# Optimization experiments

Measured on AMD Instinct MI355X. Metric: run time of the kernel, lower is better.

The kernel has to match this reference:

```python
import jax, jax.numpy as jnp
import numpy as np

DIM = 256          # channel dim
WIN = 16           # window_size
PW = WIN // 2      # permuted_window_size
N = PW * PW        # tokens per window = 64
H = 8              # num_heads
KV_DIM = DIM // 2  # compressed q/k/v dim = 128
HD = KV_DIM // H   # per-head compressed dim = 16
SCALE = (DIM // H) ** (-0.5)  # NOTE: scale uses UNcompressed head dim, as in source
B = 4096           # total windows (batch * num_windows)
NW = 64            # nw_mask; B % NW == 0


def _relative_position_index():
    coords = np.stack(np.meshgrid(np.arange(PW), np.arange(PW), indexing='ij'))  # [2,PW,PW]
    cf = coords.reshape(2, -1)                          # [2, N]
    rel = cf[:, :, None] - cf[:, None, :]               # [2, N, N]
    rel = rel.transpose(1, 2, 0).copy()                 # [N, N, 2]
    rel[:, :, 0] += PW - 1
    rel[:, :, 1] += PW - 1
    rel[:, :, 0] *= 2 * PW - 1
    return jnp.asarray(rel.sum(-1), dtype=jnp.int32)    # [N, N]


def setup_inputs() -> dict:
    key = jax.random.key(0)
    ks = jax.random.split(key, 9)
    std = 0.02
    return {
        'x': jax.random.normal(ks[0], (B, N, DIM), dtype=jnp.float32),
        'mask': jax.random.normal(ks[1], (NW, N, N), dtype=jnp.float32),
        'q_w': jax.random.normal(ks[2], (KV_DIM, DIM), dtype=jnp.float32) * std,
        'q_b': jnp.zeros((KV_DIM,), dtype=jnp.float32),
        'kv_w': jax.random.normal(ks[3], (2 * KV_DIM, DIM), dtype=jnp.float32) * std,
        'kv_b': jnp.zeros((2 * KV_DIM,), dtype=jnp.float32),
        'proj_w': jax.random.normal(ks[4], (DIM, KV_DIM), dtype=jnp.float32) * std,
        'proj_b': jnp.zeros((DIM,), dtype=jnp.float32),
        'bias_table': jax.random.normal(ks[5], ((2 * PW - 1) ** 2, H), dtype=jnp.float32) * std,
        'rel_index': _relative_position_index(),
    }


def reference(x, mask, q_w, q_b, kv_w, kv_b, proj_w, proj_b, bias_table, rel_index):
    b, n, c = x.shape
    # compressed Q and KV projections
    q = (x @ q_w.T + q_b).reshape(b, n, H, HD).transpose(0, 2, 1, 3)        # [B,H,N,HD]
    kv = (x @ kv_w.T + kv_b).reshape(b, n, 2, H, HD).transpose(2, 0, 3, 1, 4)
    k, v = kv[0], kv[1]                                                     # [B,H,N,HD]
    attn = jnp.einsum('bhnd,bhmd->bhnm', q, k) * SCALE                      # [B,H,N,N]
    # relative position bias gather
    bias = bias_table[rel_index.reshape(-1)].reshape(n, n, H).transpose(2, 0, 1)  # [H,N,N]
    attn = attn + bias[None]
    # window mask add: broadcast mask over (B//NW) window-batches and heads
    attn = attn.reshape(b // NW, NW, H, n, n) + mask[None, :, None]
    attn = attn.reshape(b, H, n, n)
    attn = jax.nn.softmax(attn, axis=-1)
    out = jnp.einsum('bhnm,bhmd->bhnd', attn, v)                            # [B,H,N,HD]
    out = out.transpose(0, 2, 1, 3).reshape(b, n, KV_DIM)
    return out @ proj_w.T + proj_b                                          # [B,N,DIM]
```

## Files before the change

### kernel.cpp

```cpp
#include <hip/hip_runtime.h>


typedef unsigned short u16;
typedef short bf16x8 __attribute__((ext_vector_type(8)));
typedef short bf16x4 __attribute__((ext_vector_type(4)));
typedef float f32x4  __attribute__((ext_vector_type(4)));

__device__ __forceinline__ f32x4 mfma_bf16(bf16x8 a, bf16x8 b, f32x4 c) {
  return __builtin_amdgcn_mfma_f32_16x16x32_bf16(a, b, c, 0, 0, 0);
}
__device__ __forceinline__ f32x4 mfma16(bf16x4 a, bf16x4 b, f32x4 c) {
#if __has_builtin(__builtin_amdgcn_mfma_f32_16x16x16bf16_1k)
  return __builtin_amdgcn_mfma_f32_16x16x16bf16_1k(a, b, c, 0, 0, 0);
#else
  f32x4 d;
  asm("v_mfma_f32_16x16x16_bf16 %0, %1, %2, %3" : "=v"(d) : "v"(a), "v"(b), "v"(c));
  return d;
#endif
}

#define SCALE_F 0.1767766952966369f
#define LOG2E_F 1.4426950408889634f
#define C2F (SCALE_F * LOG2E_F)

__device__ __forceinline__ u16 f2b(float f) {
  unsigned u = __builtin_bit_cast(unsigned, f);
  u = (u + 0x7FFFu + ((u >> 16) & 1u)) >> 16;
  return (u16)u;
}
__device__ __forceinline__ float b2f(u16 h) {
  return __builtin_bit_cast(float, (unsigned)h << 16);
}
__device__ __forceinline__ float fexp2(float x) {
#if __has_builtin(__builtin_amdgcn_exp2f)
  return __builtin_amdgcn_exp2f(x);
#else
  return __expf(x * 0.6931471805599453f);
#endif
}

#define WS_WQKV   0
#define WS_WPROJ  98304
#define WS_BIASPK 131072
#define WS_MASKPK 163840
#define WS_QKVB   425984
#define WS_TOTAL  426368

__global__ void psa_prep(const float* __restrict__ qw, const float* __restrict__ qb,
                         const float* __restrict__ kvw, const float* __restrict__ kvb,
                         const float* __restrict__ projw, const float* __restrict__ bt,
                         const int* __restrict__ ri, const float* __restrict__ mask,
                         u16* __restrict__ ws) {
  int i = blockIdx.x * 256 + threadIdx.x;
  if (i < 98304) {
    int r = i >> 8, c = i & 255;
    ws[WS_WQKV + i] = f2b(r < 128 ? qw[r * 256 + c] : kvw[(r - 128) * 256 + c]);
  } else if (i < 131072) {
    int j = i - 98304;
    ws[WS_WPROJ + j] = f2b(projw[j]);
  } else if (i < 163840) {
    int j = i - 131072;
    int t = j & 15, lane = (j >> 4) & 63, w = (j >> 10) & 3, h = j >> 12;
    int row = w * 16 + (lane & 15);
    int col = (t >> 2) * 16 + ((lane >> 4) & 3) * 4 + (t & 3);
    ws[WS_BIASPK + j] = f2b(LOG2E_F * bt[ri[row * 64 + col] * 8 + h]);
  } else if (i < 425984) {
    int j = i - 163840;
    int t = j & 15, lane = (j >> 4) & 63, w = (j >> 10) & 3, nw = j >> 12;
    int row = w * 16 + (lane & 15);
    int col = (t >> 2) * 16 + ((lane >> 4) & 3) * 4 + (t & 3);
    ws[WS_MASKPK + j] = f2b(LOG2E_F * mask[(nw * 64 + row) * 64 + col]);
  } else if (i < WS_TOTAL) {
    int j = i - 425984;
    ws[WS_QKVB + j] = f2b(j < 128 ? qb[j] : kvb[j - 128]);
  }
}

__global__ __launch_bounds__(256, 3) void psa_main(
    const float* __restrict__ x, const float* __restrict__ proj_b,
    const u16* __restrict__ ws, float* __restrict__ out) {
  __shared__ __align__(16) u16 qks[64 * 264];
  __shared__ __align__(16) u16 vsm[8 * 16 * 72];

  const int win = blockIdx.x;
  const int tid = threadIdx.x;
  const int wave = tid >> 6;
  const int lane = tid & 63;
  const int quad = lane >> 4;
  const int n16  = lane & 15;
  const int nw   = win & 63;

  const f32x4 zero4 = {0.f, 0.f, 0.f, 0.f};
  const float* xw = x + (size_t)win * 16384;

  #pragma unroll
  for (int it = 0; it < 16; ++it) {
    int idx = it * 256 + tid;
    int row = idx >> 6, c4 = (idx & 63) * 4;
    float4 v = *(const float4*)(xw + row * 256 + c4);
    bf16x4 pk;
    pk[0] = (short)f2b(v.x); pk[1] = (short)f2b(v.y);
    pk[2] = (short)f2b(v.z); pk[3] = (short)f2b(v.w);
    *(bf16x4*)&qks[row * 264 + c4] = pk;
  }
  __syncthreads();

  f32x4 acc[6][4];
  #pragma unroll
  for (int nt = 0; nt < 6; ++nt)
    #pragma unroll
    for (int mt = 0; mt < 4; ++mt) acc[nt][mt] = zero4;

  const int col0 = wave * 96;
  #pragma unroll 2
  for (int kk = 0; kk < 8; ++kk) {
    bf16x8 af[4];
    #pragma unroll
    for (int mt = 0; mt < 4; ++mt)
      af[mt] = *(const bf16x8*)&qks[(mt * 16 + n16) * 264 + kk * 32 + quad * 8];
    #pragma unroll
    for (int nt = 0; nt < 6; ++nt) {
      bf16x8 bw = *(const bf16x8*)&ws[WS_WQKV + (col0 + nt * 16 + n16) * 256 + kk * 32 + quad * 8];
      #pragma unroll
      for (int mt = 0; mt < 4; ++mt) acc[nt][mt] = mfma_bf16(af[mt], bw, acc[nt][mt]);
    }
  }
  __syncthreads();

  #pragma unroll
  for (int nt = 0; nt < 6; ++nt) {
    int col = col0 + nt * 16 + n16;
    float badd = b2f(ws[WS_QKVB + col]);
    if (col < 256) {
      #pragma unroll
      for (int mt = 0; mt < 4; ++mt)
        #pragma unroll
        for (int r = 0; r < 4; ++r)
          qks[(mt * 16 + quad * 4 + r) * 264 + col] = f2b(acc[nt][mt][r] + badd);
    } else {
      int vc = col - 256, vh = vc >> 4, vd = vc & 15;
      #pragma unroll
      for (int mt = 0; mt < 4; ++mt)
        #pragma unroll
        for (int r = 0; r < 4; ++r)
          vsm[vh * 1152 + vd * 72 + mt * 16 + quad * 4 + r] = f2b(acc[nt][mt][r] + badd);
    }
  }
  __syncthreads();

  const u16* bpk = ws + WS_BIASPK + (wave * 64 + lane) * 16;
  const u16* mpk = ws + WS_MASKPK + ((nw * 4 + wave) * 64 + lane) * 16;
  bf16x8 mm0 = *(const bf16x8*)mpk;
  bf16x8 mm1 = *(const bf16x8*)(mpk + 8);

  #pragma unroll 1
  for (int h = 0; h < 8; ++h) {
    bf16x4 qf = *(const bf16x4*)&qks[(wave * 16 + n16) * 264 + h * 16 + quad * 4];
    f32x4 s[4];
    #pragma unroll
    for (int nt = 0; nt < 4; ++nt) {
      bf16x4 kf = *(const bf16x4*)&qks[(nt * 16 + n16) * 264 + 128 + h * 16 + quad * 4];
      s[nt] = mfma16(kf, qf, zero4);
    }
    bf16x8 bm0 = *(const bf16x8*)(bpk + h * 4096);
    bf16x8 bm1 = *(const bf16x8*)(bpk + h * 4096 + 8);

    float e[4][4];
    float sum = 0.f;
    #pragma unroll
    for (int nt = 0; nt < 4; ++nt)
      #pragma unroll
      for (int r = 0; r < 4; ++r) {
        int j = nt * 4 + r;
        float bv = b2f((u16)(j < 8 ? bm0[j] : bm1[j - 8]));
        float mv = b2f((u16)(j < 8 ? mm0[j] : mm1[j - 8]));
        float ev = fexp2(s[nt][r] * C2F + (bv + mv));
        e[nt][r] = ev;
        sum += ev;
      }
    sum += __shfl_xor(sum, 16);
    sum += __shfl_xor(sum, 32);
    float rinv = __builtin_amdgcn_rcpf(sum);

    bf16x4 pf[4];
    #pragma unroll
    for (int nt = 0; nt < 4; ++nt) {
      bf16x4 t;
      #pragma unroll
      for (int r = 0; r < 4; ++r) t[r] = (short)f2b(e[nt][r]);
      pf[nt] = t;
    }
    f32x4 o = zero4;
    #pragma unroll
    for (int kt = 0; kt < 4; ++kt) {
      bf16x4 vf = *(const bf16x4*)&vsm[h * 1152 + n16 * 72 + kt * 16 + quad * 4];
      o = mfma16(vf, pf[kt], o);
    }
    bf16x4 ov;
    #pragma unroll
    for (int r = 0; r < 4; ++r) ov[r] = (short)f2b(o[r] * rinv);
    *(bf16x4*)&qks[(wave * 16 + n16) * 264 + h * 16 + quad * 4] = ov;
  }
  __syncthreads();

  f32x4 po[4][4];
  #pragma unroll
  for (int nt = 0; nt < 4; ++nt)
    #pragma unroll
    for (int mt = 0; mt < 4; ++mt) po[nt][mt] = zero4;
  #pragma unroll
  for (int ks = 0; ks < 4; ++ks) {
    bf16x8 af[4];
    #pragma unroll
    for (int mt = 0; mt < 4; ++mt)
      af[mt] = *(const bf16x8*)&qks[(mt * 16 + n16) * 264 + ks * 32 + quad * 8];
    #pragma unroll
    for (int nt = 0; nt < 4; ++nt) {
      bf16x8 bw = *(const bf16x8*)&ws[WS_WPROJ + (wave * 64 + nt * 16 + n16) * 128 + ks * 32 + quad * 8];
      #pragma unroll
      for (int mt = 0; mt < 4; ++mt) po[nt][mt] = mfma_bf16(af[mt], bw, po[nt][mt]);
    }
  }
  float* ow = out + (size_t)win * 16384;
  #pragma unroll
  for (int nt = 0; nt < 4; ++nt) {
    int coln = wave * 64 + nt * 16 + n16;
    float pb = proj_b[coln];
    #pragma unroll
    for (int mt = 0; mt < 4; ++mt)
      #pragma unroll
      for (int r = 0; r < 4; ++r)
        ow[(mt * 16 + quad * 4 + r) * 256 + coln] = po[nt][mt][r] + pb;
  }
}

extern "C" void kernel_launch(void* const* d_in, const int* in_sizes, int n_in,
                              void* d_out, int out_size, void* d_ws, size_t ws_size,
                              hipStream_t stream) {
  (void)in_sizes; (void)n_in; (void)out_size; (void)ws_size;
  const float* x    = (const float*)d_in[0];
  const float* mask = (const float*)d_in[1];
  const float* qw   = (const float*)d_in[2];
  const float* qb   = (const float*)d_in[3];
  const float* kvw  = (const float*)d_in[4];
  const float* kvb  = (const float*)d_in[5];
  const float* pw   = (const float*)d_in[6];
  const float* pb   = (const float*)d_in[7];
  const float* bt   = (const float*)d_in[8];
  const int*   ri   = (const int*)d_in[9];
  u16* ws = (u16*)d_ws;

  psa_prep<<<(WS_TOTAL + 255) / 256, 256, 0, stream>>>(qw, qb, kvw, kvb, pw, bt, ri, mask, ws);
  psa_main<<<4096, 256, 0, stream>>>(x, pb, ws, (float*)d_out);
}
```

Measured before the change: 566.2 us.

## Transpose MFMA operands so projection outputs store as packed vectors

Swaps the A/B operand roles in the QKV and output-projection MFMAs so each lane holds four consecutive output channels for one token. Q/K stores to LDS become packed 8-byte writes, and the final output becomes float4 global stores instead of scattered scalar stores. The weight tiles are also interleaved across waves (wave + i*4). Smaller changes: the attention head loop is unrolled by two, the softmax sum uses a tree reduction, and f2b uses the library bf16 conversion. The V stores stay scalar, now with a different LDS address pattern that may cause bank conflicts.

```diff
diff --git a/kernel.cpp b/kernel.cpp
--- a/kernel.cpp
+++ b/kernel.cpp
@@ -1,4 +1,5 @@
 #include <hip/hip_runtime.h>
+#include <hip/hip_bf16.h>
 
 
 typedef unsigned short u16;
@@ -24,9 +25,7 @@
 #define C2F (SCALE_F * LOG2E_F)
 
 __device__ __forceinline__ u16 f2b(float f) {
-  unsigned u = __builtin_bit_cast(unsigned, f);
-  u = (u + 0x7FFFu + ((u >> 16) & 1u)) >> 16;
-  return (u16)u;
+  return __builtin_bit_cast(u16, __float2bfloat16(f));
 }
 __device__ __forceinline__ float b2f(u16 h) {
   return __builtin_bit_cast(float, (unsigned)h << 16);
@@ -107,43 +106,48 @@
 
   f32x4 acc[6][4];
   #pragma unroll
-  for (int nt = 0; nt < 6; ++nt)
-    #pragma unroll
-    for (int mt = 0; mt < 4; ++mt) acc[nt][mt] = zero4;
-
-  const int col0 = wave * 96;
+  for (int i = 0; i < 6; ++i)
+    #pragma unroll
+    for (int nt = 0; nt < 4; ++nt) acc[i][nt] = zero4;
+
   #pragma unroll 2
   for (int kk = 0; kk < 8; ++kk) {
-    bf16x8 af[4];
-    #pragma unroll
-    for (int mt = 0; mt < 4; ++mt)
-      af[mt] = *(const bf16x8*)&qks[(mt * 16 + n16) * 264 + kk * 32 + quad * 8];
-    #pragma unroll
-    for (int nt = 0; nt < 6; ++nt) {
-      bf16x8 bw = *(const bf16x8*)&ws[WS_WQKV + (col0 + nt * 16 + n16) * 256 + kk * 32 + quad * 8];
-      #pragma unroll
-      for (int mt = 0; mt < 4; ++mt) acc[nt][mt] = mfma_bf16(af[mt], bw, acc[nt][mt]);
-    }
-  }
-  __syncthreads();
-
-  #pragma unroll
-  for (int nt = 0; nt < 6; ++nt) {
-    int col = col0 + nt * 16 + n16;
-    float badd = b2f(ws[WS_QKVB + col]);
-    if (col < 256) {
-      #pragma unroll
-      for (int mt = 0; mt < 4; ++mt)
+    bf16x8 xf[4];
+    #pragma unroll
+    for (int nt = 0; nt < 4; ++nt)
+      xf[nt] = *(const bf16x8*)&qks[(nt * 16 + n16) * 264 + kk * 32 + quad * 8];
+    #pragma unroll
+    for (int i = 0; i < 6; ++i) {
+      int mt = wave + i * 4;
+      bf16x8 wf = *(const bf16x8*)&ws[WS_WQKV + (mt * 16 + n16) * 256 + kk * 32 + quad * 8];
+      #pragma unroll
+      for (int nt = 0; nt < 4; ++nt) acc[i][nt] = mfma_bf16(wf, xf[nt], acc[i][nt]);
+    }
+  }
+  __syncthreads();
+
+  #pragma unroll
+  for (int i = 0; i < 6; ++i) {
+    int mt = wave + i * 4;
+    bf16x4 bq = *(const bf16x4*)&ws[WS_QKVB + mt * 16 + quad * 4];
+    float ba[4];
+    #pragma unroll
+    for (int r = 0; r < 4; ++r) ba[r] = b2f((u16)bq[r]);
+    if (i < 4) {
+      #pragma unroll
+      for (int nt = 0; nt < 4; ++nt) {
+        bf16x4 pk;
+        #pragma unroll
+        for (int r = 0; r < 4; ++r) pk[r] = (short)f2b(acc[i][nt][r] + ba[r]);
+        *(bf16x4*)&qks[(nt * 16 + n16) * 264 + mt * 16 + quad * 4] = pk;
+      }
+    } else {
+      #pragma unroll
+      for (int nt = 0; nt < 4; ++nt)
         #pragma unroll
         for (int r = 0; r < 4; ++r)
-          qks[(mt * 16 + quad * 4 + r) * 264 + col] = f2b(acc[nt][mt][r] + badd);
-    } else {
-      int vc = col - 256, vh = vc >> 4, vd = vc & 15;
-      #pragma unroll
-      for (int mt = 0; mt < 4; ++mt)
-        #pragma unroll
-        for (int r = 0; r < 4; ++r)
-          vsm[vh * 1152 + vd * 72 + mt * 16 + quad * 4 + r] = f2b(acc[nt][mt][r] + badd);
+          vsm[(mt - 16) * 1152 + (quad * 4 + r) * 72 + nt * 16 + n16] =
+              f2b(acc[i][nt][r] + ba[r]);
     }
   }
   __syncthreads();
@@ -153,7 +157,7 @@
   bf16x8 mm0 = *(const bf16x8*)mpk;
   bf16x8 mm1 = *(const bf16x8*)(mpk + 8);
 
-  #pragma unroll 1
+  #pragma unroll 2
   for (int h = 0; h < 8; ++h) {
     bf16x4 qf = *(const bf16x4*)&qks[(wave * 16 + n16) * 264 + h * 16 + quad * 4];
     f32x4 s[4];
@@ -166,18 +170,19 @@
     bf16x8 bm1 = *(const bf16x8*)(bpk + h * 4096 + 8);
 
     float e[4][4];
-    float sum = 0.f;
-    #pragma unroll
-    for (int nt = 0; nt < 4; ++nt)
+    float psum[4];
+    #pragma unroll
+    for (int nt = 0; nt < 4; ++nt) {
       #pragma unroll
       for (int r = 0; r < 4; ++r) {
         int j = nt * 4 + r;
         float bv = b2f((u16)(j < 8 ? bm0[j] : bm1[j - 8]));
         float mv = b2f((u16)(j < 8 ? mm0[j] : mm1[j - 8]));
-        float ev = fexp2(s[nt][r] * C2F + (bv + mv));
-        e[nt][r] = ev;
-        sum += ev;
+        e[nt][r] = fexp2(s[nt][r] * C2F + (bv + mv));
       }
+      psum[nt] = (e[nt][0] + e[nt][1]) + (e[nt][2] + e[nt][3]);
+    }
+    float sum = (psum[0] + psum[1]) + (psum[2] + psum[3]);
     sum += __shfl_xor(sum, 16);
     sum += __shfl_xor(sum, 32);
     float rinv = __builtin_amdgcn_rcpf(sum);
@@ -205,32 +210,37 @@
 
   f32x4 po[4][4];
   #pragma unroll
-  for (int nt = 0; nt < 4; ++nt)
-    #pragma unroll
-    for (int mt = 0; mt < 4; ++mt) po[nt][mt] = zero4;
+  for (int i = 0; i < 4; ++i)
+    #pragma unroll
+    for (int nt = 0; nt < 4; ++nt) po[i][nt] = zero4;
   #pragma unroll
   for (int ks = 0; ks < 4; ++ks) {
-    bf16x8 af[4];
-    #pragma unroll
-    for (int mt = 0; mt < 4; ++mt)
-      af[mt] = *(const bf16x8*)&qks[(mt * 16 + n16) * 264 + ks * 32 + quad * 8];
-    #pragma unroll
-    for (int nt = 0; nt < 4; ++nt) {
-      bf16x8 bw = *(const bf16x8*)&ws[WS_WPROJ + (wave * 64 + nt * 16 + n16) * 128 + ks * 32 + quad * 8];
-      #pragma unroll
-      for (int mt = 0; mt < 4; ++mt) po[nt][mt] = mfma_bf16(af[mt], bw, po[nt][mt]);
+    bf16x8 of[4];
+    #pragma unroll
+    for (int nt = 0; nt < 4; ++nt)
+      of[nt] = *(const bf16x8*)&qks[(nt * 16 + n16) * 264 + ks * 32 + quad * 8];
+    #pragma unroll
+    for (int i = 0; i < 4; ++i) {
+      bf16x8 wf = *(const bf16x8*)&ws[WS_WPROJ + ((wave * 4 + i) * 16 + n16) * 128 + ks * 32 + quad * 8];
+      #pragma unroll
+      for (int nt = 0; nt < 4; ++nt) po[i][nt] = mfma_bf16(wf, of[nt], po[i][nt]);
     }
   }
   float* ow = out + (size_t)win * 16384;
   #pragma unroll
-  for (int nt = 0; nt < 4; ++nt) {
-    int coln = wave * 64 + nt * 16 + n16;
-    float pb = proj_b[coln];
-    #pragma unroll
-    for (int mt = 0; mt < 4; ++mt)
-      #pragma unroll
-      for (int r = 0; r < 4; ++r)
-        ow[(mt * 16 + quad * 4 + r) * 256 + coln] = po[nt][mt][r] + pb;
+  for (int i = 0; i < 4; ++i) {
+    int cbase = (wave * 4 + i) * 16 + quad * 4;
+    float4 pbv = *(const float4*)(proj_b + cbase);
+    #pragma unroll
+    for (int nt = 0; nt < 4; ++nt) {
+      int token = nt * 16 + n16;
+      float4 st;
+      st.x = po[i][nt][0] + pbv.x;
+      st.y = po[i][nt][1] + pbv.y;
+      st.z = po[i][nt][2] + pbv.z;
+      st.w = po[i][nt][3] + pbv.w;
+      *(float4*)(ow + token * 256 + cbase) = st;
+    }
   }
 }
 
```

New measurement: 580.1 us. 1.02x slower.
